# Optimization experiments

Measured on AMD Instinct MI355X. Metric: run time of the kernel, lower is better.

The kernel has to match this reference:

```python
import jax, jax.numpy as jnp
import numpy as np

B = 512          # batch
V = 6890         # SMPL vertices
NB = 10          # num_betas
NJ = 24          # joints (root + 23 body)
# canonical SMPL kinematic tree (parents[0] = -1 for root)
PARENTS = np.array([-1,0,0,0,1,2,3,4,5,6,7,8,9,9,9,12,13,14,16,17,18,19,20,21], dtype=np.int32)


def rodrigues(rot_vecs):
    """Axis-angle [N,3] -> rotation matrices [N,3,3] (matches batch_rodrigues)."""
    angle = jnp.linalg.norm(rot_vecs + 1e-8, axis=1, keepdims=True)  # [N,1]
    rot_dir = rot_vecs / angle
    cos = jnp.cos(angle)[:, :, None]  # [N,1,1]
    sin = jnp.sin(angle)[:, :, None]
    rx, ry, rz = rot_dir[:, 0], rot_dir[:, 1], rot_dir[:, 2]
    zeros = jnp.zeros_like(rx)
    K = jnp.stack([zeros, -rz, ry,
                   rz, zeros, -rx,
                   -ry, rx, zeros], axis=1).reshape(-1, 3, 3)
    I = jnp.eye(3, dtype=rot_vecs.dtype)
    return I[None] + sin * K + (1.0 - cos) * jnp.matmul(K, K)


def setup_inputs() -> dict:
    key = jax.random.key(0)
    ks = jax.random.split(key, 8)
    betas = jnp.concatenate([jnp.ones((B, 1), jnp.float32),
                             0.5 * jax.random.normal(ks[0], (B, NB), jnp.float32)], axis=1)
    body_pose = 0.3 * jax.random.normal(ks[1], (B, 3 * (NJ - 1)), jnp.float32)
    global_orient = 0.3 * jax.random.normal(ks[2], (B, 3), jnp.float32)
    transl = jax.random.normal(ks[3], (B, 3), jnp.float32)
    shapedirs = 0.01 * jax.random.normal(ks[4], (V, 3, NB), jnp.float32)
    v_template = jax.random.normal(ks[5], (V, 3), jnp.float32)
    Jr = jax.random.uniform(ks[6], (NJ, V), jnp.float32)
    Jr = Jr / jnp.sum(Jr, axis=1, keepdims=True)
    W = jax.random.uniform(ks[7], (V, NJ), jnp.float32)
    W = W / jnp.sum(W, axis=1, keepdims=True)             # convex skinning weights
    return dict(betas=betas, body_pose=body_pose, global_orient=global_orient,
                transl=transl, shapedirs=shapedirs, v_template=v_template,
                J_regressor=Jr, lbs_weights=W)


def reference(betas, body_pose, global_orient, transl,
              shapedirs, v_template, J_regressor, lbs_weights):
    dt = v_template.dtype
    blend = jnp.einsum('bl,mkl->bmk', betas[:, 1:], shapedirs)            # [B,V,3]
    v_shaped = (v_template[None] + blend) * betas[:, 0][:, None, None]    # [B,V,3]
    J = jnp.einsum('bik,ji->bjk', v_shaped, J_regressor)                  # [B,NJ,3]
    # ---- updatePose: axis-angle -> rotmats
    full_pose = jnp.concatenate([global_orient, body_pose], axis=1)       # [B,NJ*3]
    rot_mats = rodrigues(full_pose.reshape(-1, 3)).reshape(-1, NJ, 3, 3)  # [B,NJ,3,3]
    # ---- kinematic chain (batch_rigid_transform)
    rel = J.at[:, 1:].add(-J[:, PARENTS[1:]])                             # rel joint offsets
    T_local = jnp.concatenate([rot_mats, rel[..., None]], axis=3)         # [B,NJ,3,4]
    bottom = jnp.broadcast_to(jnp.array([0, 0, 0, 1], dt), (rot_mats.shape[0], NJ, 1, 4))
    T_local = jnp.concatenate([T_local, bottom], axis=2)                  # [B,NJ,4,4]
    chain = [T_local[:, 0]]
    for i in range(1, NJ):  # fixed 24-node tree
        chain.append(jnp.matmul(chain[PARENTS[i]], T_local[:, i]))
    transforms = jnp.stack(chain, axis=1)                                 # [B,NJ,4,4]
    J_transformed = transforms[:, :, :3, 3]                               # [B,NJ,3]
    # relative transforms: subtract rotated rest joint from translation column
    init_t = jnp.einsum('bnij,bnj->bni', transforms[:, :, :3, :3], J)
    A = transforms.at[:, :, :3, 3].add(-init_t)                           # [B,NJ,4,4]
    # ---- skinning: T = W @ A, apply to homogeneous verts
    T = jnp.einsum('vn,bnij->bvij', lbs_weights, A)                       # [B,V,4,4]
    verts = (jnp.einsum('bvij,bvj->bvi', T[:, :, :3, :3], v_shaped)
             + T[:, :, :3, 3] + transl[:, None])                          # [B,V,3]
    return verts, J_transformed
```

## Files before the change

kernel.cpp:

```cpp
#include <hip/hip_runtime.h>

#define BATCH 512
#define V 6890
#define NJ 24
#define VH (V/2)

#define SD_N (V*30)
#define VT_N (V*3)
#define W_N  (V*24)
#define TOT_PK (SD_N+VT_N+W_N)

#define A_OFF   0
#define BS_OFF  147456
#define JT_OFF  155648
#define JS_OFF  155720
#define PK_OFF  156672

__device__ const int d_par[NJ] = {-1,0,0,0,1,2,3,4,5,6,7,8,9,9,9,12,13,14,16,17,18,19,20,21};

__global__ __launch_bounds__(256) void prep_k(
    const float* __restrict__ sd, const float* __restrict__ vt, const float* __restrict__ W,
    float* __restrict__ dst)
{
  int i = blockIdx.x*256 + threadIdx.x;
  if (i >= TOT_PK) return;
  float val;
  if (i < SD_N){ int j=i/V, v=i-j*V; val = sd[v*30+j]; }
  else if (i < SD_N+VT_N){ int o=i-SD_N; int j=o/V, v=o-j*V; val = vt[v*3+j]; }
  else { int o=i-SD_N-VT_N; int j=o/V, v=o-j*V; val = W[v*24+j]; }
  dst[i] = val;
}

__global__ __launch_bounds__(256) void jreg_k(
    const float* __restrict__ Jr, const float* __restrict__ pk,
    float* __restrict__ JTo, float* __restrict__ JSo)
{
  const int j = blockIdx.x;
  const int c = blockIdx.y;
  const int t = threadIdx.x;
  const float* __restrict__ col = (c<3) ? (pk + (30+c)*V) : (pk + (c-3)*V);
  float acc = 0.f;
  for (int v=t; v<V; v+=256){
    acc = fmaf(Jr[j*V+v], col[v], acc);
  }
  __shared__ float red[256];
  red[t]=acc; __syncthreads();
  for (int s=128;s>0;s>>=1){ if(t<s) red[t]+=red[t+s]; __syncthreads(); }
  if (t==0){
    if (c<3) JTo[j*3+c]=red[0];
    else {
      int idx=c-3, k=idx/10, l=idx-10*(idx/10);
      JSo[(j*3+k)*10+l] = red[0];
    }
  }
}

__global__ __launch_bounds__(64) void batch_k(
    const float* __restrict__ betas, const float* __restrict__ body_pose,
    const float* __restrict__ go, const float* __restrict__ transl,
    const float* __restrict__ JT, const float* __restrict__ JS,
    float* __restrict__ A, float* __restrict__ bsc, float* __restrict__ jout)
{
  const int b = blockIdx.x;
  const int t = threadIdx.x;
  __shared__ float lb[11];
  __shared__ float lJ[72];
  __shared__ float lR[NJ*9];
  __shared__ float lL[NJ*12];
  __shared__ float lW[NJ*12];
  if (t < 11) lb[t] = betas[b*11+t];
  __syncthreads();
  const float b0 = lb[0];
  for (int idx=t; idx<72; idx+=64){
    float s = JT[idx];
    #pragma unroll
    for (int l=0;l<10;l++) s = fmaf(lb[1+l], JS[idx*10+l], s);
    lJ[idx] = b0*s;
  }
  if (t==0) bsc[b*16] = b0;
  if (t>=1 && t<11) bsc[b*16+t] = b0*lb[t];
  if (t<3) bsc[b*16+11+t] = transl[b*3+t];
  if (t < NJ){
    float p0,p1,p2;
    if (t==0){ p0=go[b*3+0]; p1=go[b*3+1]; p2=go[b*3+2]; }
    else { int o=b*69+(t-1)*3; p0=body_pose[o]; p1=body_pose[o+1]; p2=body_pose[o+2]; }
    float a0=p0+1e-8f, a1=p1+1e-8f, a2=p2+1e-8f;
    float angle = sqrtf(a0*a0+a1*a1+a2*a2);
    float inv = 1.0f/angle;
    float rx=p0*inv, ry=p1*inv, rz=p2*inv;
    float sn = sinf(angle), cs = cosf(angle), mc = 1.0f-cs;
    float K[9] = {0.f,-rz,ry, rz,0.f,-rx, -ry,rx,0.f};
    float KK[9];
    #pragma unroll
    for (int r=0;r<3;r++)
      #pragma unroll
      for (int c=0;c<3;c++)
        KK[r*3+c] = K[r*3+0]*K[0+c] + K[r*3+1]*K[3+c] + K[r*3+2]*K[6+c];
    #pragma unroll
    for (int e=0;e<9;e++){
      float ident = (e==0||e==4||e==8)?1.0f:0.0f;
      lR[t*9+e] = ident + sn*K[e] + mc*KK[e];
    }
  }
  __syncthreads();
  for (int idx=t; idx<288; idx+=64){
    int j = idx/12, rc = idx-12*j, r = rc>>2, c = rc&3;
    float val;
    if (c<3) val = lR[j*9 + r*3 + c];
    else {
      int p = (j==0) ? 0 : d_par[j];
      val = (j==0) ? lJ[r] : (lJ[j*3+r] - lJ[p*3+r]);
    }
    lL[idx] = val;
  }
  __syncthreads();
  if (t<12) lW[t] = lL[t];
  __syncthreads();
  for (int i=1;i<NJ;i++){
    if (t<12){
      int p = d_par[i];
      int r = t>>2, c = t&3;
      float s = lW[p*12+r*4+0]*lL[i*12+0+c]
              + lW[p*12+r*4+1]*lL[i*12+4+c]
              + lW[p*12+r*4+2]*lL[i*12+8+c];
      if (c==3) s += lW[p*12+r*4+3];
      lW[i*12+t] = s;
    }
    __syncthreads();
  }
  for (int idx=t; idx<72; idx+=64){
    int j=idx/3, k=idx-3*j;
    jout[b*72+idx] = lW[j*12+k*4+3];
  }
  const int g = b>>2, q = b&3;
  float* __restrict__ Ab = A + g*1152 + q*12;
  for (int idx=t; idx<288; idx+=64){
    int n=idx/12, rc=idx-12*n, r=rc>>2, c=rc&3;
    float val = lW[n*12+rc];
    if (c==3){
      val -= lW[n*12+r*4+0]*lJ[n*3+0] + lW[n*12+r*4+1]*lJ[n*3+1] + lW[n*12+r*4+2]*lJ[n*3+2];
    }
    Ab[n*48 + rc] = val;
  }
}

__global__ __launch_bounds__(256) void main_k(
    const float* __restrict__ A, const float* __restrict__ bsc,
    const float2* __restrict__ pk, float* __restrict__ out)
{
  const int vh = blockIdx.x*256 + threadIdx.x;
  if (vh >= VH) return;
  const int bg = blockIdx.y;
  const float* __restrict__ Ag = A + bg*1152;
  const float* __restrict__ bs = bsc + bg*64;

  const float2 vt0 = pk[30*VH + vh];
  const float2 vt1 = pk[31*VH + vh];
  const float2 vt2 = pk[32*VH + vh];

  float2 vs[4][3];
#pragma unroll
  for (int q=0;q<4;q++){
    const float b0 = bs[q*16];
    vs[q][0] = make_float2(b0*vt0.x, b0*vt0.y);
    vs[q][1] = make_float2(b0*vt1.x, b0*vt1.y);
    vs[q][2] = make_float2(b0*vt2.x, b0*vt2.y);
  }
#pragma unroll
  for (int l=0;l<10;l++){
    const float2 s0 = pk[(0*10+l)*VH + vh];
    const float2 s1 = pk[(1*10+l)*VH + vh];
    const float2 s2 = pk[(2*10+l)*VH + vh];
#pragma unroll
    for (int q=0;q<4;q++){
      const float c = bs[q*16+1+l];
      vs[q][0].x = fmaf(c, s0.x, vs[q][0].x); vs[q][0].y = fmaf(c, s0.y, vs[q][0].y);
      vs[q][1].x = fmaf(c, s1.x, vs[q][1].x); vs[q][1].y = fmaf(c, s1.y, vs[q][1].y);
      vs[q][2].x = fmaf(c, s2.x, vs[q][2].x); vs[q][2].y = fmaf(c, s2.y, vs[q][2].y);
    }
  }

  float y[4][6];
#pragma unroll
  for (int q=0;q<4;q++)
#pragma unroll
    for (int i=0;i<6;i++) y[q][i] = 0.f;

#pragma unroll 4
  for (int n=0;n<NJ;n++){
    const float2 w = pk[(33+n)*VH + vh];
#pragma unroll
    for (int q=0;q<4;q++){
      const float* __restrict__ an = Ag + n*48 + q*12;
      float tt;
      tt = fmaf(an[2], vs[q][2].x, fmaf(an[1], vs[q][1].x, fmaf(an[0], vs[q][0].x, an[3])));
      y[q][0] = fmaf(w.x, tt, y[q][0]);
      tt = fmaf(an[2], vs[q][2].y, fmaf(an[1], vs[q][1].y, fmaf(an[0], vs[q][0].y, an[3])));
      y[q][1] = fmaf(w.y, tt, y[q][1]);
      tt = fmaf(an[6], vs[q][2].x, fmaf(an[5], vs[q][1].x, fmaf(an[4], vs[q][0].x, an[7])));
      y[q][2] = fmaf(w.x, tt, y[q][2]);
      tt = fmaf(an[6], vs[q][2].y, fmaf(an[5], vs[q][1].y, fmaf(an[4], vs[q][0].y, an[7])));
      y[q][3] = fmaf(w.y, tt, y[q][3]);
      tt = fmaf(an[10], vs[q][2].x, fmaf(an[9], vs[q][1].x, fmaf(an[8], vs[q][0].x, an[11])));
      y[q][4] = fmaf(w.x, tt, y[q][4]);
      tt = fmaf(an[10], vs[q][2].y, fmaf(an[9], vs[q][1].y, fmaf(an[8], vs[q][0].y, an[11])));
      y[q][5] = fmaf(w.y, tt, y[q][5]);
    }
  }

  const int v0 = 2*vh;
#pragma unroll
  for (int q=0;q<4;q++){
    const float t0 = bs[q*16+11], t1 = bs[q*16+12], t2 = bs[q*16+13];
    const int b = bg*4 + q;
    float2* __restrict__ o2 = (float2*)(out + (b*V + v0)*3);
    o2[0] = make_float2(y[q][0]+t0, y[q][2]+t1);
    o2[1] = make_float2(y[q][4]+t2, y[q][1]+t0);
    o2[2] = make_float2(y[q][3]+t1, y[q][5]+t2);
  }
}

extern "C" void kernel_launch(void* const* d_in, const int* in_sizes, int n_in,
                              void* d_out, int out_size, void* d_ws, size_t ws_size,
                              hipStream_t stream)
{
  const float* betas     = (const float*)d_in[0];
  const float* body_pose = (const float*)d_in[1];
  const float* go        = (const float*)d_in[2];
  const float* transl    = (const float*)d_in[3];
  const float* sdirs     = (const float*)d_in[4];
  const float* vtempl    = (const float*)d_in[5];
  const float* Jr        = (const float*)d_in[6];
  const float* lw        = (const float*)d_in[7];
  float* wsf = (float*)d_ws;
  float* out = (float*)d_out;

  hipLaunchKernelGGL(prep_k, dim3((TOT_PK+255)/256), dim3(256), 0, stream,
                     sdirs, vtempl, lw, wsf+PK_OFF);
  hipLaunchKernelGGL(jreg_k, dim3(24,33), dim3(256), 0, stream,
                     Jr, wsf+PK_OFF, wsf+JT_OFF, wsf+JS_OFF);
  hipLaunchKernelGGL(batch_k, dim3(BATCH), dim3(64), 0, stream,
                     betas, body_pose, go, transl, wsf+JT_OFF, wsf+JS_OFF,
                     wsf+A_OFF, wsf+BS_OFF, out + BATCH*V*3);
  hipLaunchKernelGGL(main_k, dim3((VH+255)/256, BATCH/4), dim3(256), 0, stream,
                     wsf+A_OFF, wsf+BS_OFF, (const float2*)(wsf+PK_OFF), out);
}
```

Measured before the change: 148.8 us.

## Fuse prep and joint regression kernels, halve batch grouping in skinning kernel

Merges the transpose/pack kernel with joint regression into one launch. The regression now reads the original layouts directly, keeps 33 accumulators per thread and reduces them with wave shuffles, so it no longer depends on the packed buffer. The main skinning kernel now processes 2 batch items per thread instead of 4 and sets a launch-bounds occupancy hint of 8 to cut register pressure. The cost is that per-vertex shape-dir and weight data is reloaded twice as often across batch groups.

```diff
diff --git a/kernel.cpp b/kernel.cpp
--- a/kernel.cpp
+++ b/kernel.cpp
@@ -9,6 +9,7 @@
 #define VT_N (V*3)
 #define W_N  (V*24)
 #define TOT_PK (SD_N+VT_N+W_N)
+#define PREP_BLOCKS ((TOT_PK+255)/256)
 
 #define A_OFF   0
 #define BS_OFF  147456
@@ -18,40 +19,59 @@
 
 __device__ const int d_par[NJ] = {-1,0,0,0,1,2,3,4,5,6,7,8,9,9,9,12,13,14,16,17,18,19,20,21};
 
-__global__ __launch_bounds__(256) void prep_k(
+__global__ __launch_bounds__(256) void prepjreg_k(
     const float* __restrict__ sd, const float* __restrict__ vt, const float* __restrict__ W,
-    float* __restrict__ dst)
-{
-  int i = blockIdx.x*256 + threadIdx.x;
-  if (i >= TOT_PK) return;
-  float val;
-  if (i < SD_N){ int j=i/V, v=i-j*V; val = sd[v*30+j]; }
-  else if (i < SD_N+VT_N){ int o=i-SD_N; int j=o/V, v=o-j*V; val = vt[v*3+j]; }
-  else { int o=i-SD_N-VT_N; int j=o/V, v=o-j*V; val = W[v*24+j]; }
-  dst[i] = val;
-}
-
-__global__ __launch_bounds__(256) void jreg_k(
-    const float* __restrict__ Jr, const float* __restrict__ pk,
-    float* __restrict__ JTo, float* __restrict__ JSo)
-{
-  const int j = blockIdx.x;
-  const int c = blockIdx.y;
+    const float* __restrict__ Jr,
+    float* __restrict__ dst, float* __restrict__ JTo, float* __restrict__ JSo)
+{
+  __shared__ float red[4*33];
+  const int bid = blockIdx.x;
+  if (bid < PREP_BLOCKS){
+    int i = bid*256 + threadIdx.x;
+    if (i >= TOT_PK) return;
+    float val;
+    if (i < SD_N){ int j=i/V, v=i-j*V; val = sd[v*30+j]; }
+    else if (i < SD_N+VT_N){ int o=i-SD_N; int j=o/V, v=o-j*V; val = vt[v*3+j]; }
+    else { int o=i-SD_N-VT_N; int j=o/V, v=o-j*V; val = W[v*24+j]; }
+    dst[i] = val;
+    return;
+  }
+  const int j = bid - PREP_BLOCKS;
   const int t = threadIdx.x;
-  const float* __restrict__ col = (c<3) ? (pk + (30+c)*V) : (pk + (c-3)*V);
-  float acc = 0.f;
+  float acc[33];
+#pragma unroll
+  for (int m=0;m<33;m++) acc[m]=0.f;
   for (int v=t; v<V; v+=256){
-    acc = fmaf(Jr[j*V+v], col[v], acc);
-  }
-  __shared__ float red[256];
-  red[t]=acc; __syncthreads();
-  for (int s=128;s>0;s>>=1){ if(t<s) red[t]+=red[t+s]; __syncthreads(); }
-  if (t==0){
-    if (c<3) JTo[j*3+c]=red[0];
-    else {
-      int idx=c-3, k=idx/10, l=idx-10*(idx/10);
-      JSo[(j*3+k)*10+l] = red[0];
-    }
+    const float jr = Jr[j*V+v];
+    const float* __restrict__ vp = vt + v*3;
+    acc[0] = fmaf(jr, vp[0], acc[0]);
+    acc[1] = fmaf(jr, vp[1], acc[1]);
+    acc[2] = fmaf(jr, vp[2], acc[2]);
+    const float2* __restrict__ sp = (const float2*)(sd + v*30);
+#pragma unroll
+    for (int m=0;m<15;m++){
+      const float2 s = sp[m];
+      acc[3+2*m]   = fmaf(jr, s.x, acc[3+2*m]);
+      acc[3+2*m+1] = fmaf(jr, s.y, acc[3+2*m+1]);
+    }
+  }
+  const int lane = t & 63, wid = t >> 6;
+#pragma unroll
+  for (int m=0;m<33;m++){
+    float x = acc[m];
+    x += __shfl_xor(x, 1);
+    x += __shfl_xor(x, 2);
+    x += __shfl_xor(x, 4);
+    x += __shfl_xor(x, 8);
+    x += __shfl_xor(x, 16);
+    x += __shfl_xor(x, 32);
+    if (lane == 0) red[wid*33+m] = x;
+  }
+  __syncthreads();
+  if (t < 33){
+    const float s = red[t] + red[33+t] + red[66+t] + red[99+t];
+    if (t < 3) JTo[j*3+t] = s;
+    else       JSo[j*30 + (t-3)] = s;
   }
 }
 
@@ -132,35 +152,35 @@
     int j=idx/3, k=idx-3*j;
     jout[b*72+idx] = lW[j*12+k*4+3];
   }
-  const int g = b>>2, q = b&3;
-  float* __restrict__ Ab = A + g*1152 + q*12;
+  const int g = b>>1, q = b&1;
+  float* __restrict__ Ab = A + g*576 + q*12;
   for (int idx=t; idx<288; idx+=64){
     int n=idx/12, rc=idx-12*n, r=rc>>2, c=rc&3;
     float val = lW[n*12+rc];
     if (c==3){
       val -= lW[n*12+r*4+0]*lJ[n*3+0] + lW[n*12+r*4+1]*lJ[n*3+1] + lW[n*12+r*4+2]*lJ[n*3+2];
     }
-    Ab[n*48 + rc] = val;
-  }
-}
-
-__global__ __launch_bounds__(256) void main_k(
+    Ab[n*24 + rc] = val;
+  }
+}
+
+__global__ __launch_bounds__(256, 8) void main_k(
     const float* __restrict__ A, const float* __restrict__ bsc,
     const float2* __restrict__ pk, float* __restrict__ out)
 {
   const int vh = blockIdx.x*256 + threadIdx.x;
   if (vh >= VH) return;
   const int bg = blockIdx.y;
-  const float* __restrict__ Ag = A + bg*1152;
-  const float* __restrict__ bs = bsc + bg*64;
+  const float* __restrict__ Ag = A + bg*576;
+  const float* __restrict__ bs = bsc + bg*32;
 
   const float2 vt0 = pk[30*VH + vh];
   const float2 vt1 = pk[31*VH + vh];
   const float2 vt2 = pk[32*VH + vh];
 
-  float2 vs[4][3];
-#pragma unroll
-  for (int q=0;q<4;q++){
+  float2 vs[2][3];
+#pragma unroll
+  for (int q=0;q<2;q++){
     const float b0 = bs[q*16];
     vs[q][0] = make_float2(b0*vt0.x, b0*vt0.y);
     vs[q][1] = make_float2(b0*vt1.x, b0*vt1.y);
@@ -172,7 +192,7 @@
     const float2 s1 = pk[(1*10+l)*VH + vh];
     const float2 s2 = pk[(2*10+l)*VH + vh];
 #pragma unroll
-    for (int q=0;q<4;q++){
+    for (int q=0;q<2;q++){
       const float c = bs[q*16+1+l];
       vs[q][0].x = fmaf(c, s0.x, vs[q][0].x); vs[q][0].y = fmaf(c, s0.y, vs[q][0].y);
       vs[q][1].x = fmaf(c, s1.x, vs[q][1].x); vs[q][1].y = fmaf(c, s1.y, vs[q][1].y);
@@ -180,9 +200,9 @@
     }
   }
 
-  float y[4][6];
-#pragma unroll
-  for (int q=0;q<4;q++)
+  float y[2][6];
+#pragma unroll
+  for (int q=0;q<2;q++)
 #pragma unroll
     for (int i=0;i<6;i++) y[q][i] = 0.f;
 
@@ -190,8 +210,8 @@
   for (int n=0;n<NJ;n++){
     const float2 w = pk[(33+n)*VH + vh];
 #pragma unroll
-    for (int q=0;q<4;q++){
-      const float* __restrict__ an = Ag + n*48 + q*12;
+    for (int q=0;q<2;q++){
+      const float* __restrict__ an = Ag + n*24 + q*12;
       float tt;
       tt = fmaf(an[2], vs[q][2].x, fmaf(an[1], vs[q][1].x, fmaf(an[0], vs[q][0].x, an[3])));
       y[q][0] = fmaf(w.x, tt, y[q][0]);
@@ -210,9 +230,9 @@
 
   const int v0 = 2*vh;
 #pragma unroll
-  for (int q=0;q<4;q++){
+  for (int q=0;q<2;q++){
     const float t0 = bs[q*16+11], t1 = bs[q*16+12], t2 = bs[q*16+13];
-    const int b = bg*4 + q;
+    const int b = bg*2 + q;
     float2* __restrict__ o2 = (float2*)(out + (b*V + v0)*3);
     o2[0] = make_float2(y[q][0]+t0, y[q][2]+t1);
     o2[1] = make_float2(y[q][4]+t2, y[q][1]+t0);
@@ -235,13 +255,11 @@
   float* wsf = (float*)d_ws;
   float* out = (float*)d_out;
 
-  hipLaunchKernelGGL(prep_k, dim3((TOT_PK+255)/256), dim3(256), 0, stream,
-                     sdirs, vtempl, lw, wsf+PK_OFF);
-  hipLaunchKernelGGL(jreg_k, dim3(24,33), dim3(256), 0, stream,
-                     Jr, wsf+PK_OFF, wsf+JT_OFF, wsf+JS_OFF);
+  hipLaunchKernelGGL(prepjreg_k, dim3(PREP_BLOCKS + 24), dim3(256), 0, stream,
+                     sdirs, vtempl, lw, Jr, wsf+PK_OFF, wsf+JT_OFF, wsf+JS_OFF);
   hipLaunchKernelGGL(batch_k, dim3(BATCH), dim3(64), 0, stream,
                      betas, body_pose, go, transl, wsf+JT_OFF, wsf+JS_OFF,
                      wsf+A_OFF, wsf+BS_OFF, out + BATCH*V*3);
-  hipLaunchKernelGGL(main_k, dim3((VH+255)/256, BATCH/4), dim3(256), 0, stream,
+  hipLaunchKernelGGL(main_k, dim3((VH+255)/256, BATCH/2), dim3(256), 0, stream,
                      wsf+A_OFF, wsf+BS_OFF, (const float2*)(wsf+PK_OFF), out);
 }
```

Result: no change. 149.9 us (+0.7%).
